# Kernel optimization log

Hardware: AMD Instinct MI355X
Metric: run time of the kernel (lower is better)

Reference implementation:

```python
import jax, jax.numpy as jnp
import numpy as np

B, D, E, K = 8192, 1024, 8, 5  # batch, in_dim, num_size_classes, num_depth_classes
H = max(64, D)                 # hidden = max(64, in_dim)
EPS = 1e-8


def ordinal_logits_to_probs(logits, num_classes):
    # logits: [B, K-1] cumulative ordinal logits -> [B, K] class probs
    q = jax.nn.sigmoid(logits)
    probs = jnp.concatenate(
        [1.0 - q[:, :1], q[:, :-1] - q[:, 1:], q[:, -1:]], axis=1
    )  # [B, K]
    probs = jnp.clip(probs, EPS)
    return probs / jnp.clip(probs.sum(axis=1, keepdims=True), EPS)


def setup_inputs() -> dict:
    key = jax.random.key(0)
    kx, ks, k1, k2 = jax.random.split(key, 4)
    x = jax.random.normal(kx, (B, D), dtype=jnp.float32)
    size_idx = jax.random.randint(ks, (B,), 0, E, dtype=jnp.int64)
    # per-expert 2-layer MLP params: Linear(D,H) -> ReLU -> Linear(H,K-1)
    W1 = jax.random.normal(k1, (E, D, H), dtype=jnp.float32) / np.sqrt(D)
    b1 = jnp.zeros((E, H), dtype=jnp.float32)
    W2 = jax.random.normal(k2, (E, H, K - 1), dtype=jnp.float32) / np.sqrt(H)
    b2 = jnp.zeros((E, K - 1), dtype=jnp.float32)
    return {"x": x, "size_idx": size_idx, "W1": W1, "b1": b1, "W2": W2, "b2": b2}


def reference(x, size_idx, W1, b1, W2, b2):
    # Hard routing: each token gets the output of expert size_idx[b].
    # Dense all-expert compute + per-token select (same math as mask/gather/scatter,
    # dropout is inference-mode identity).
    h = jax.nn.relu(jnp.einsum('bd,edh->beh', x, W1) + b1)      # [B, E, H]
    all_logits = jnp.einsum('beh,ehk->bek', h, W2) + b2          # [B, E, K-1]
    idx = size_idx.astype(jnp.int32)[:, None, None]              # [B, 1, 1]
    logits = jnp.take_along_axis(all_logits, idx, axis=1)[:, 0]  # [B, K-1]
    probs = ordinal_logits_to_probs(logits, K)                   # [B, K]
    return logits, probs
```

## Files before the change

### kernel.cpp

```cpp
#include <hip/hip_runtime.h>
#include <cstdint>
#include <cstddef>

#define Bn 8192
#define Dn 1024
#define Hn 1024
#define En 8
#define MT 128
#define MTILES (PERM_N / MT)
#define PERM_N (Bn + En * MT)
#define NB 16

#define NXB 4096
#define NWB 2048
#define XB0 1
#define WB0 (XB0 + NXB)
#define TOTB (WB0 + NWB)

typedef unsigned short u16;
typedef __bf16 bf16x8 __attribute__((ext_vector_type(8)));
typedef float f32x4 __attribute__((ext_vector_type(4)));
typedef unsigned short ushort8 __attribute__((ext_vector_type(8)));

__device__ __forceinline__ u16 f2bf(float f) {
  unsigned int u = __float_as_uint(f);
  unsigned int r = u + 0x7fffu + ((u >> 16) & 1u);
  return (u16)(r >> 16);
}

__device__ __forceinline__ void gld16(const void* g, void* l) {
  __builtin_amdgcn_global_load_lds(
      (const __attribute__((address_space(1))) void*)g,
      (__attribute__((address_space(3))) void*)l, 16, 0, 0);
}

#define PIPE_BARRIER_VM4() do {                    \
    asm volatile("" ::: "memory");                 \
    __builtin_amdgcn_s_waitcnt(0x0F74);            \
    __builtin_amdgcn_s_barrier();                  \
    asm volatile("" ::: "memory");                 \
  } while (0)
#define PIPE_BARRIER_VM0() do {                    \
    asm volatile("" ::: "memory");                 \
    __builtin_amdgcn_s_waitcnt(0x0F70);            \
    __builtin_amdgcn_s_barrier();                  \
    asm volatile("" ::: "memory");                 \
  } while (0)

__global__ __launch_bounds__(256) void prep_k(
    const float* __restrict__ x, const int* __restrict__ sidx,
    const float* __restrict__ W1,
    u16* __restrict__ xb, u16* __restrict__ w1t,
    int* __restrict__ off, int* __restrict__ perm) {
  int bid = blockIdx.x;
  int t = threadIdx.x;

  if (bid == 0) {
    __shared__ int hist[4][En];
    __shared__ int base[4][En];
    __shared__ int eoff[En + 1];
    int wv = t >> 6;
    if (t < 4 * En) ((int*)hist)[t] = 0;
#pragma unroll
    for (int i = 0; i < PERM_N / 256; i++) perm[t + i * 256] = -1;
    __syncthreads();
    int e32[32], r32[32];
#pragma unroll
    for (int i = 0; i < 32; i++) {
      int e = sidx[t + i * 256];
      e32[i] = e;
      r32[i] = atomicAdd(&hist[wv][e], 1);
    }
    __syncthreads();
    if (t < En) {
      int s = 0;
      for (int w = 0; w < 4; w++) { base[w][t] = s; s += hist[w][t]; }
      hist[0][t] = s;
    }
    __syncthreads();
    if (t == 0) {
      int o = 0;
      for (int e = 0; e < En; e++) {
        eoff[e] = o; off[e] = o;
        o += (hist[0][e] + MT - 1) & ~(MT - 1);
      }
      eoff[En] = o; off[En] = o;
    }
    __syncthreads();
#pragma unroll
    for (int i = 0; i < 32; i++) {
      int e = e32[i];
      perm[eoff[e] + base[wv][e] + r32[i]] = t + i * 256;
    }
  } else if (bid < WB0) {
    size_t idx = ((size_t)(bid - XB0) * 256 + t) * 8;
    const float* src = x + idx;
    float4 a = *(const float4*)src;
    float4 b = *(const float4*)(src + 4);
    ushort8 o;
    o[0] = f2bf(a.x); o[1] = f2bf(a.y); o[2] = f2bf(a.z); o[3] = f2bf(a.w);
    o[4] = f2bf(b.x); o[5] = f2bf(b.y); o[6] = f2bf(b.z); o[7] = f2bf(b.w);
    *(ushort8*)(xb + idx) = o;
  } else {
    __shared__ float tile[64][65];
    int wb = bid - WB0;
    int e = wb >> 8;
    int k0 = ((wb >> 4) & 15) * 64;
    int n0 = (wb & 15) * 64;
    int c4 = (t & 15) * 4;
    int r0 = t >> 4;
    const float* src = W1 + ((size_t)e << 20) + (size_t)k0 * Hn + n0;
#pragma unroll
    for (int i = 0; i < 4; i++) {
      int r = r0 + i * 16;
      float4 v = *(const float4*)(src + (size_t)r * Hn + c4);
      tile[r][c4 + 0] = v.x; tile[r][c4 + 1] = v.y;
      tile[r][c4 + 2] = v.z; tile[r][c4 + 3] = v.w;
    }
    __syncthreads();
    u16* dst = w1t + ((size_t)e << 20) + (size_t)n0 * Dn + k0;
#pragma unroll
    for (int i = 0; i < 4; i++) {
      int h = r0 + i * 16;
      ushort4 o;
      o.x = f2bf(tile[c4 + 0][h]);
      o.y = f2bf(tile[c4 + 1][h]);
      o.z = f2bf(tile[c4 + 2][h]);
      o.w = f2bf(tile[c4 + 3][h]);
      *(ushort4*)(dst + (size_t)h * Dn + c4) = o;
    }
  }
}

__global__ __launch_bounds__(256) void gemm_k(
    const u16* __restrict__ xb, const u16* __restrict__ w1t,
    const float* __restrict__ b1, const float* __restrict__ w2,
    const int* __restrict__ off, const int* __restrict__ perm,
    float* __restrict__ partials) {
  __shared__ u16 As[3][4096];
  __shared__ u16 Bs[3][4096];

  int n0 = blockIdx.x * 128;
  int row0 = blockIdx.y * MT;
  if (row0 >= off[En]) return;
  int e = 0;
  while (row0 >= off[e + 1]) e++;

  int tid = threadIdx.x;
  int lane = tid & 63, w = tid >> 6;
  int wm = w >> 1, wn = w & 1;

  int srow = lane >> 2;
  int slot = lane & 3;
  int scol = (slot ^ ((srow >> 1) & 3)) * 8;
  const u16* aG[2]; const u16* bG[2];
  int lOff[2];
#pragma unroll
  for (int j = 0; j < 2; j++) {
    int rl = 32 * w + 16 * j + srow;
    int tok = perm[row0 + rl];
    if (tok < 0) tok = 0;
    aG[j] = xb + ((size_t)tok << 10) + scol;
    bG[j] = w1t + ((size_t)e << 20) + (size_t)(n0 + rl) * Dn + scol;
    lOff[j] = (32 * w + 16 * j) * 32;
  }

  f32x4 acc[4][4];
#pragma unroll
  for (int i = 0; i < 4; i++)
#pragma unroll
    for (int j = 0; j < 4; j++)
      acc[i][j] = (f32x4){0.f, 0.f, 0.f, 0.f};

  int fr = lane & 15;
  int qf = lane >> 4;
  int qs = (qf ^ ((fr >> 1) & 3)) * 8;
  int offA[4], offB[4];
#pragma unroll
  for (int i = 0; i < 4; i++)
    offA[i] = (wm * 64 + i * 16 + fr) * 32 + qs;
#pragma unroll
  for (int j = 0; j < 4; j++)
    offB[j] = (wn * 64 + j * 16 + fr) * 32 + qs;

#pragma unroll
  for (int it = 0; it < 2; it++) {
    int ko = it * 32;
    gld16(aG[0] + ko, (u16*)As[it] + lOff[0]);
    gld16(aG[1] + ko, (u16*)As[it] + lOff[1]);
    gld16(bG[0] + ko, (u16*)Bs[it] + lOff[0]);
    gld16(bG[1] + ko, (u16*)Bs[it] + lOff[1]);
  }

#pragma unroll
  for (int i = 0; i < 31; i++) {
    PIPE_BARRIER_VM4();
    if (i + 2 < 32) {
      int s = (i + 2) % 3;
      int ko = (i + 2) * 32;
      gld16(aG[0] + ko, (u16*)As[s] + lOff[0]);
      gld16(aG[1] + ko, (u16*)As[s] + lOff[1]);
      gld16(bG[0] + ko, (u16*)Bs[s] + lOff[0]);
      gld16(bG[1] + ko, (u16*)Bs[s] + lOff[1]);
    }
    const u16* Ab = (const u16*)As[i % 3];
    const u16* Bb = (const u16*)Bs[i % 3];
    bf16x8 af[4], bfr[4];
#pragma unroll
    for (int ii = 0; ii < 4; ii++) af[ii] = *(const bf16x8*)(Ab + offA[ii]);
#pragma unroll
    for (int jj = 0; jj < 4; jj++) bfr[jj] = *(const bf16x8*)(Bb + offB[jj]);
#pragma unroll
    for (int ii = 0; ii < 4; ii++)
#pragma unroll
      for (int jj = 0; jj < 4; jj++)
        acc[ii][jj] = __builtin_amdgcn_mfma_f32_16x16x32_bf16(af[ii], bfr[jj], acc[ii][jj], 0, 0, 0);
  }
  {
    PIPE_BARRIER_VM0();
    const u16* Ab = (const u16*)As[31 % 3];
    const u16* Bb = (const u16*)Bs[31 % 3];
    bf16x8 af[4], bfr[4];
#pragma unroll
    for (int ii = 0; ii < 4; ii++) af[ii] = *(const bf16x8*)(Ab + offA[ii]);
#pragma unroll
    for (int jj = 0; jj < 4; jj++) bfr[jj] = *(const bf16x8*)(Bb + offB[jj]);
#pragma unroll
    for (int ii = 0; ii < 4; ii++)
#pragma unroll
      for (int jj = 0; jj < 4; jj++)
        acc[ii][jj] = __builtin_amdgcn_mfma_f32_16x16x32_bf16(af[ii], bfr[jj], acc[ii][jj], 0, 0, 0);
  }

  int fq = lane >> 4;
  float4 w2v[4]; float b1v[4];
#pragma unroll
  for (int j = 0; j < 4; j++) {
    int col = n0 + wn * 64 + j * 16 + fr;
    w2v[j] = *(const float4*)(w2 + ((size_t)e * Hn + col) * 4);
    b1v[j] = b1[(size_t)e * Hn + col];
  }
  int chunk = blockIdx.x * 2 + wn;
#pragma unroll
  for (int i = 0; i < 4; i++) {
    int rbase = wm * 64 + i * 16 + fq * 4;
#pragma unroll
    for (int r = 0; r < 4; r++) {
      float s0 = 0.f, s1 = 0.f, s2 = 0.f, s3 = 0.f;
#pragma unroll
      for (int j = 0; j < 4; j++) {
        float h = acc[i][j][r] + b1v[j];
        h = fmaxf(h, 0.f);
        s0 = fmaf(h, w2v[j].x, s0);
        s1 = fmaf(h, w2v[j].y, s1);
        s2 = fmaf(h, w2v[j].z, s2);
        s3 = fmaf(h, w2v[j].w, s3);
      }
#pragma unroll
      for (int m = 1; m < 16; m <<= 1) {
        s0 += __shfl_xor(s0, m);
        s1 += __shfl_xor(s1, m);
        s2 += __shfl_xor(s2, m);
        s3 += __shfl_xor(s3, m);
      }
      if (fr == 0) {
        int row = row0 + rbase + r;
        *(float4*)(partials + ((size_t)row * NB + chunk) * 4) =
            make_float4(s0, s1, s2, s3);
      }
    }
  }
}

__global__ void probs_k(const float* __restrict__ partials,
                        const int* __restrict__ perm, const int* __restrict__ off,
                        const int* __restrict__ sidx, const float* __restrict__ b2,
                        float* __restrict__ out) {
  int p = blockIdx.x * blockDim.x + threadIdx.x;
  if (p >= off[En]) return;
  int tok = perm[p];
  if (tok < 0) return;
  int e = sidx[tok];
  float s0 = 0.f, s1 = 0.f, s2 = 0.f, s3 = 0.f;
#pragma unroll
  for (int nb = 0; nb < NB; nb++) {
    float4 v = *(const float4*)(partials + ((size_t)p * NB + nb) * 4);
    s0 += v.x; s1 += v.y; s2 += v.z; s3 += v.w;
  }
  float l0 = s0 + b2[e * 4 + 0];
  float l1 = s1 + b2[e * 4 + 1];
  float l2 = s2 + b2[e * 4 + 2];
  float l3 = s3 + b2[e * 4 + 3];
  out[tok * 4 + 0] = l0; out[tok * 4 + 1] = l1;
  out[tok * 4 + 2] = l2; out[tok * 4 + 3] = l3;
  float q0 = 1.f / (1.f + expf(-l0));
  float q1 = 1.f / (1.f + expf(-l1));
  float q2 = 1.f / (1.f + expf(-l2));
  float q3 = 1.f / (1.f + expf(-l3));
  const float eps = 1e-8f;
  float p0 = fmaxf(1.f - q0, eps);
  float p1 = fmaxf(q0 - q1, eps);
  float p2 = fmaxf(q1 - q2, eps);
  float p3 = fmaxf(q2 - q3, eps);
  float p4 = fmaxf(q3, eps);
  float s = p0 + p1 + p2 + p3 + p4;
  float inv = 1.f / fmaxf(s, eps);
  float* pr = out + (size_t)Bn * 4 + (size_t)tok * 5;
  pr[0] = p0 * inv; pr[1] = p1 * inv; pr[2] = p2 * inv;
  pr[3] = p3 * inv; pr[4] = p4 * inv;
}

extern "C" void kernel_launch(void* const* d_in, const int* in_sizes, int n_in,
                              void* d_out, int out_size, void* d_ws, size_t ws_size,
                              hipStream_t stream) {
  const float* x  = (const float*)d_in[0];
  const int* sidx = (const int*)d_in[1];
  const float* W1 = (const float*)d_in[2];
  const float* b1 = (const float*)d_in[3];
  const float* W2 = (const float*)d_in[4];
  const float* b2 = (const float*)d_in[5];
  float* out = (float*)d_out;

  uint8_t* w = (uint8_t*)d_ws;
  int* off  = (int*)(w + 64);
  int* perm = (int*)(w + 512);
  u16* xb      = (u16*)(w + 40960);
  u16* w1t     = (u16*)(w + 40960 + 16777216);
  float* parts = (float*)(w + 40960 + 2 * 16777216);

  prep_k<<<TOTB, 256, 0, stream>>>(x, sidx, W1, xb, w1t, off, perm);
  gemm_k<<<dim3(Hn / 128, MTILES), 256, 0, stream>>>(xb, w1t, b1, W2, off, perm, parts);
  probs_k<<<(PERM_N + 255) / 256, 256, 0, stream>>>(parts, perm, off, sidx, b2, out);
}
```

Baseline: 156.0 us.

## Deepen GEMM LDS pipeline to four stages and process two tiles per block

Result: slower. 168.2 us (+7.9%).

```diff
diff --git a/kernel.cpp b/kernel.cpp
--- a/kernel.cpp
+++ b/kernel.cpp
@@ -10,6 +10,7 @@
 #define MTILES (PERM_N / MT)
 #define PERM_N (Bn + En * MT)
 #define NB 16
+#define GBLK 288
 
 #define NXB 4096
 #define NWB 2048
@@ -34,15 +35,9 @@
       (__attribute__((address_space(3))) void*)l, 16, 0, 0);
 }
 
-#define PIPE_BARRIER_VM4() do {                    \
+#define PIPE_BARRIER(imm) do {                     \
     asm volatile("" ::: "memory");                 \
-    __builtin_amdgcn_s_waitcnt(0x0F74);            \
-    __builtin_amdgcn_s_barrier();                  \
-    asm volatile("" ::: "memory");                 \
-  } while (0)
-#define PIPE_BARRIER_VM0() do {                    \
-    asm volatile("" ::: "memory");                 \
-    __builtin_amdgcn_s_waitcnt(0x0F70);            \
+    __builtin_amdgcn_s_waitcnt(imm);               \
     __builtin_amdgcn_s_barrier();                  \
     asm volatile("" ::: "memory");                 \
   } while (0)
@@ -137,15 +132,10 @@
     const float* __restrict__ b1, const float* __restrict__ w2,
     const int* __restrict__ off, const int* __restrict__ perm,
     float* __restrict__ partials) {
-  __shared__ u16 As[3][4096];
-  __shared__ u16 Bs[3][4096];
-
-  int n0 = blockIdx.x * 128;
-  int row0 = blockIdx.y * MT;
-  if (row0 >= off[En]) return;
-  int e = 0;
-  while (row0 >= off[e + 1]) e++;
-
+  __shared__ u16 As[4][4096];
+  __shared__ u16 Bs[4][4096];
+
+  int b = blockIdx.x;
   int tid = threadIdx.x;
   int lane = tid & 63, w = tid >> 6;
   int wm = w >> 1, wn = w & 1;
@@ -153,25 +143,6 @@
   int srow = lane >> 2;
   int slot = lane & 3;
   int scol = (slot ^ ((srow >> 1) & 3)) * 8;
-  const u16* aG[2]; const u16* bG[2];
-  int lOff[2];
-#pragma unroll
-  for (int j = 0; j < 2; j++) {
-    int rl = 32 * w + 16 * j + srow;
-    int tok = perm[row0 + rl];
-    if (tok < 0) tok = 0;
-    aG[j] = xb + ((size_t)tok << 10) + scol;
-    bG[j] = w1t + ((size_t)e << 20) + (size_t)(n0 + rl) * Dn + scol;
-    lOff[j] = (32 * w + 16 * j) * 32;
-  }
-
-  f32x4 acc[4][4];
-#pragma unroll
-  for (int i = 0; i < 4; i++)
-#pragma unroll
-    for (int j = 0; j < 4; j++)
-      acc[i][j] = (f32x4){0.f, 0.f, 0.f, 0.f};
-
   int fr = lane & 15;
   int qf = lane >> 4;
   int qs = (qf ^ ((fr >> 1) & 3)) * 8;
@@ -183,90 +154,108 @@
   for (int j = 0; j < 4; j++)
     offB[j] = (wn * 64 + j * 16 + fr) * 32 + qs;
 
-#pragma unroll
-  for (int it = 0; it < 2; it++) {
-    int ko = it * 32;
-    gld16(aG[0] + ko, (u16*)As[it] + lOff[0]);
-    gld16(aG[1] + ko, (u16*)As[it] + lOff[1]);
-    gld16(bG[0] + ko, (u16*)Bs[it] + lOff[0]);
-    gld16(bG[1] + ko, (u16*)Bs[it] + lOff[1]);
-  }
-
-#pragma unroll
-  for (int i = 0; i < 31; i++) {
-    PIPE_BARRIER_VM4();
-    if (i + 2 < 32) {
-      int s = (i + 2) % 3;
-      int ko = (i + 2) * 32;
-      gld16(aG[0] + ko, (u16*)As[s] + lOff[0]);
-      gld16(aG[1] + ko, (u16*)As[s] + lOff[1]);
-      gld16(bG[0] + ko, (u16*)Bs[s] + lOff[0]);
-      gld16(bG[1] + ko, (u16*)Bs[s] + lOff[1]);
-    }
-    const u16* Ab = (const u16*)As[i % 3];
-    const u16* Bb = (const u16*)Bs[i % 3];
-    bf16x8 af[4], bfr[4];
-#pragma unroll
-    for (int ii = 0; ii < 4; ii++) af[ii] = *(const bf16x8*)(Ab + offA[ii]);
-#pragma unroll
-    for (int jj = 0; jj < 4; jj++) bfr[jj] = *(const bf16x8*)(Bb + offB[jj]);
-#pragma unroll
-    for (int ii = 0; ii < 4; ii++)
-#pragma unroll
-      for (int jj = 0; jj < 4; jj++)
-        acc[ii][jj] = __builtin_amdgcn_mfma_f32_16x16x32_bf16(af[ii], bfr[jj], acc[ii][jj], 0, 0, 0);
-  }
-  {
-    PIPE_BARRIER_VM0();
-    const u16* Ab = (const u16*)As[31 % 3];
-    const u16* Bb = (const u16*)Bs[31 % 3];
-    bf16x8 af[4], bfr[4];
-#pragma unroll
-    for (int ii = 0; ii < 4; ii++) af[ii] = *(const bf16x8*)(Ab + offA[ii]);
-#pragma unroll
-    for (int jj = 0; jj < 4; jj++) bfr[jj] = *(const bf16x8*)(Bb + offB[jj]);
-#pragma unroll
-    for (int ii = 0; ii < 4; ii++)
-#pragma unroll
-      for (int jj = 0; jj < 4; jj++)
-        acc[ii][jj] = __builtin_amdgcn_mfma_f32_16x16x32_bf16(af[ii], bfr[jj], acc[ii][jj], 0, 0, 0);
-  }
-
-  int fq = lane >> 4;
-  float4 w2v[4]; float b1v[4];
-#pragma unroll
-  for (int j = 0; j < 4; j++) {
-    int col = n0 + wn * 64 + j * 16 + fr;
-    w2v[j] = *(const float4*)(w2 + ((size_t)e * Hn + col) * 4);
-    b1v[j] = b1[(size_t)e * Hn + col];
-  }
-  int chunk = blockIdx.x * 2 + wn;
-#pragma unroll
-  for (int i = 0; i < 4; i++) {
-    int rbase = wm * 64 + i * 16 + fq * 4;
-#pragma unroll
-    for (int r = 0; r < 4; r++) {
-      float s0 = 0.f, s1 = 0.f, s2 = 0.f, s3 = 0.f;
-#pragma unroll
-      for (int j = 0; j < 4; j++) {
-        float h = acc[i][j][r] + b1v[j];
-        h = fmaxf(h, 0.f);
-        s0 = fmaf(h, w2v[j].x, s0);
-        s1 = fmaf(h, w2v[j].y, s1);
-        s2 = fmaf(h, w2v[j].z, s2);
-        s3 = fmaf(h, w2v[j].w, s3);
+  int offEn = off[En];
+
+#pragma unroll 1
+  for (int ti = 0; ti < 2; ti++) {
+    int t = b + ti * GBLK;
+    int n0 = (t & 7) * 128;
+    int row0 = (t >> 3) * MT;
+    if (row0 >= offEn) continue;
+    int e = 0;
+    while (row0 >= off[e + 1]) e++;
+
+    const u16* aG[2]; const u16* bG[2];
+    int lOff[2];
+#pragma unroll
+    for (int j = 0; j < 2; j++) {
+      int rl = 32 * w + 16 * j + srow;
+      int tok = perm[row0 + rl];
+      if (tok < 0) tok = 0;
+      aG[j] = xb + ((size_t)tok << 10) + scol;
+      bG[j] = w1t + ((size_t)e << 20) + (size_t)(n0 + rl) * Dn + scol;
+      lOff[j] = (32 * w + 16 * j) * 32;
+    }
+
+    f32x4 acc[4][4];
+#pragma unroll
+    for (int i = 0; i < 4; i++)
+#pragma unroll
+      for (int j = 0; j < 4; j++)
+        acc[i][j] = (f32x4){0.f, 0.f, 0.f, 0.f};
+
+#pragma unroll
+    for (int it = 0; it < 3; it++) {
+      int ko = it * 32;
+      gld16(aG[0] + ko, (u16*)As[it] + lOff[0]);
+      gld16(aG[1] + ko, (u16*)As[it] + lOff[1]);
+      gld16(bG[0] + ko, (u16*)Bs[it] + lOff[0]);
+      gld16(bG[1] + ko, (u16*)Bs[it] + lOff[1]);
+    }
+
+#pragma unroll
+    for (int i = 0; i < 32; i++) {
+      if (i <= 28)      PIPE_BARRIER(0x0F7C);
+      else if (i == 29) PIPE_BARRIER(0x0F78);
+      else if (i == 30) PIPE_BARRIER(0x0F74);
+      else              PIPE_BARRIER(0x0F70);
+      if (i + 3 < 32) {
+        int s = (i + 3) & 3;
+        int ko = (i + 3) * 32;
+        gld16(aG[0] + ko, (u16*)As[s] + lOff[0]);
+        gld16(aG[1] + ko, (u16*)As[s] + lOff[1]);
+        gld16(bG[0] + ko, (u16*)Bs[s] + lOff[0]);
+        gld16(bG[1] + ko, (u16*)Bs[s] + lOff[1]);
       }
-#pragma unroll
-      for (int m = 1; m < 16; m <<= 1) {
-        s0 += __shfl_xor(s0, m);
-        s1 += __shfl_xor(s1, m);
-        s2 += __shfl_xor(s2, m);
-        s3 += __shfl_xor(s3, m);
-      }
-      if (fr == 0) {
-        int row = row0 + rbase + r;
-        *(float4*)(partials + ((size_t)row * NB + chunk) * 4) =
-            make_float4(s0, s1, s2, s3);
+      const u16* Ab = (const u16*)As[i & 3];
+      const u16* Bb = (const u16*)Bs[i & 3];
+      bf16x8 af[4], bfr[4];
+#pragma unroll
+      for (int ii = 0; ii < 4; ii++) af[ii] = *(const bf16x8*)(Ab + offA[ii]);
+#pragma unroll
+      for (int jj = 0; jj < 4; jj++) bfr[jj] = *(const bf16x8*)(Bb + offB[jj]);
+#pragma unroll
+      for (int ii = 0; ii < 4; ii++)
+#pragma unroll
+        for (int jj = 0; jj < 4; jj++)
+          acc[ii][jj] = __builtin_amdgcn_mfma_f32_16x16x32_bf16(af[ii], bfr[jj], acc[ii][jj], 0, 0, 0);
+    }
+
+    float4 w2v[4]; float b1v[4];
+#pragma unroll
+    for (int j = 0; j < 4; j++) {
+      int col = n0 + wn * 64 + j * 16 + fr;
+      w2v[j] = *(const float4*)(w2 + ((size_t)e * Hn + col) * 4);
+      b1v[j] = b1[(size_t)e * Hn + col];
+    }
+    int chunk = (t & 7) * 2 + wn;
+#pragma unroll
+    for (int i = 0; i < 4; i++) {
+      int rbase = wm * 64 + i * 16 + qf * 4;
+#pragma unroll
+      for (int r = 0; r < 4; r++) {
+        float s0 = 0.f, s1 = 0.f, s2 = 0.f, s3 = 0.f;
+#pragma unroll
+        for (int j = 0; j < 4; j++) {
+          float h = acc[i][j][r] + b1v[j];
+          h = fmaxf(h, 0.f);
+          s0 = fmaf(h, w2v[j].x, s0);
+          s1 = fmaf(h, w2v[j].y, s1);
+          s2 = fmaf(h, w2v[j].z, s2);
+          s3 = fmaf(h, w2v[j].w, s3);
+        }
+#pragma unroll
+        for (int m = 1; m < 16; m <<= 1) {
+          s0 += __shfl_xor(s0, m);
+          s1 += __shfl_xor(s1, m);
+          s2 += __shfl_xor(s2, m);
+          s3 += __shfl_xor(s3, m);
+        }
+        if (fr == 0) {
+          int row = row0 + rbase + r;
+          *(float4*)(partials + ((size_t)row * NB + chunk) * 4) =
+              make_float4(s0, s1, s2, s3);
+        }
       }
     }
   }
@@ -329,6 +318,6 @@
   float* parts = (float*)(w + 40960 + 2 * 16777216);
 
   prep_k<<<TOTB, 256, 0, stream>>>(x, sidx, W1, xb, w1t, off, perm);
-  gemm_k<<<dim3(Hn / 128, MTILES), 256, 0, stream>>>(xb, w1t, b1, W2, off, perm, parts);
+  gemm_k<<<GBLK, 256, 0, stream>>>(xb, w1t, b1, W2, off, perm, parts);
   probs_k<<<(PERM_N + 255) / 256, 256, 0, stream>>>(parts, perm, off, sidx, b2, out);
 }
```
